# Performance work log

Measured on AMD Instinct MI355X. Metric: run time of the kernel, lower is better.

The kernel has to match this reference:

```python
import jax, jax.numpy as jnp
import numpy as np

HS = 4096
NIN = 17   # RFSIZE*RFSIZE + ADDINPUT + NBACTIONS = 9 + 4 + 4
NACT = 4


def setup_inputs() -> dict:
    key = jax.random.key(0)
    ks = jax.random.split(key, 10)
    return {
        "inputs": jax.random.normal(ks[0], (1, NIN), jnp.float32),
        "hidden": jax.random.normal(ks[1], (1, HS), jnp.float32) * 0.1,
        "hebb": jnp.zeros((HS, HS), jnp.float32),
        "et": jnp.zeros((HS, HS), jnp.float32),
        "pw": jnp.zeros((HS, HS), jnp.float32),
        # i2h Linear(17 -> hs)
        "i2h_w": jax.random.normal(ks[2], (HS, NIN), jnp.float32) * (1.0 / np.sqrt(NIN)),
        "i2h_b": jax.random.normal(ks[3], (HS,), jnp.float32) * 0.01,
        # plastic recurrent params: 0.01 * rand, eta = 0.01 * ones(1)
        "w": 0.01 * jax.random.uniform(ks[4], (HS, HS), jnp.float32),
        "alpha": 0.01 * jax.random.uniform(ks[5], (HS, HS), jnp.float32),
        "eta": 0.01 * jnp.ones((1,), jnp.float32),
        # output heads
        "h2o_w": jax.random.normal(ks[6], (NACT, HS), jnp.float32) * (1.0 / np.sqrt(HS)),
        "h2o_b": jax.random.normal(ks[7], (NACT,), jnp.float32) * 0.01,
        "h2v_w": jax.random.normal(ks[8], (1, HS), jnp.float32) * (1.0 / np.sqrt(HS)),
        "h2v_b": jax.random.normal(ks[9], (1,), jnp.float32) * 0.01,
    }


def reference(inputs, hidden, hebb, et, pw,
              i2h_w, i2h_b, w, alpha, eta,
              h2o_w, h2o_b, h2v_w, h2v_b):
    # type='plastic', rule='hebb', clp=0, addpw=0
    # hactiv = tanh(i2h(inputs) + hidden @ (w + alpha * hebb))
    pre = inputs @ i2h_w.T + i2h_b + hidden @ (w + alpha * hebb)  # [1, HS]
    hactiv = jnp.tanh(pre)
    activout = hactiv @ h2o_w.T + h2o_b   # [1, NBACTIONS]
    valueout = hactiv @ h2v_w.T + h2v_b   # [1, 1]
    # deltahebb = outer(hidden[0], hactiv[0])  (batch 1, matches torch.bmm(...)[0])
    deltahebb = hidden[0][:, None] * hactiv[0][None, :]  # [HS, HS]
    hebb_new = (1.0 - eta) * hebb + eta * deltahebb       # eta shape (1,) broadcasts
    # hidden <- hactiv; et, pw untouched for this type
    return activout, valueout, hactiv, hebb_new, et, pw
```

## Files before the change

### kernel.cpp

```cpp
#include <hip/hip_runtime.h>
#include <math.h>

#define HS 4096
#define NIN 17
#define ROW_CHUNKS 512
#define ROWS_PER_CHUNK (HS / ROW_CHUNKS)

__global__ __launch_bounds__(256) void matvec_partial_k(
    const float* __restrict__ hidden, const float* __restrict__ w,
    const float* __restrict__ alpha, const float* __restrict__ hebb,
    float* __restrict__ partial) {
  const int j4 = blockIdx.x * blockDim.x + threadIdx.x;
  const int row0 = blockIdx.y * ROWS_PER_CHUNK;
  const size_t base = (size_t)row0 * (HS / 4) + j4;
  const float4* wp = reinterpret_cast<const float4*>(w) + base;
  const float4* ap = reinterpret_cast<const float4*>(alpha) + base;
  const float4* bp = reinterpret_cast<const float4*>(hebb) + base;
  float4 acc = make_float4(0.f, 0.f, 0.f, 0.f);
#pragma unroll
  for (int r = 0; r < ROWS_PER_CHUNK; ++r) {
    const float h = hidden[row0 + r];
    const float4 wv = wp[(size_t)r * (HS / 4)];
    const float4 av = ap[(size_t)r * (HS / 4)];
    const float4 bv = bp[(size_t)r * (HS / 4)];
    acc.x = fmaf(h, fmaf(av.x, bv.x, wv.x), acc.x);
    acc.y = fmaf(h, fmaf(av.y, bv.y, wv.y), acc.y);
    acc.z = fmaf(h, fmaf(av.z, bv.z, wv.z), acc.z);
    acc.w = fmaf(h, fmaf(av.w, bv.w, wv.w), acc.w);
  }
  reinterpret_cast<float4*>(partial)[(size_t)blockIdx.y * (HS / 4) + j4] = acc;
}

__global__ __launch_bounds__(256) void finalize_k(
    const float* __restrict__ partial, const float* __restrict__ inputs,
    const float* __restrict__ i2h_w, const float* __restrict__ i2h_b,
    float* __restrict__ out_hactiv) {
  const int j = blockIdx.x * blockDim.x + threadIdx.x;
  float s = i2h_b[j];
#pragma unroll
  for (int k = 0; k < NIN; ++k) s = fmaf(inputs[k], i2h_w[j * NIN + k], s);
  float r = 0.f;
  for (int c = 0; c < ROW_CHUNKS; ++c) r += partial[(size_t)c * HS + j];
  out_hactiv[j] = tanhf(s + r);
}

__global__ __launch_bounds__(256) void heads_k(
    const float* __restrict__ hactiv, const float* __restrict__ h2o_w,
    const float* __restrict__ h2o_b, const float* __restrict__ h2v_w,
    const float* __restrict__ h2v_b, float* __restrict__ out) {
  const int r = blockIdx.x;
  const float* wrow = (r < 4) ? (h2o_w + (size_t)r * HS) : h2v_w;
  float s = 0.f;
  for (int j = threadIdx.x; j < HS; j += 256) s = fmaf(hactiv[j], wrow[j], s);
  __shared__ float red[256];
  red[threadIdx.x] = s;
  __syncthreads();
  for (int off = 128; off > 0; off >>= 1) {
    if (threadIdx.x < off) red[threadIdx.x] += red[threadIdx.x + off];
    __syncthreads();
  }
  if (threadIdx.x == 0) {
    const float b = (r < 4) ? h2o_b[r] : h2v_b[0];
    out[r] = red[0] + b;
  }
}

__global__ __launch_bounds__(256) void elementwise_k(
    const float* __restrict__ hebb, const float* __restrict__ hidden,
    const float* __restrict__ hactiv, const float* __restrict__ eta,
    const float* __restrict__ et, const float* __restrict__ pw,
    float* __restrict__ out_hebb, float* __restrict__ out_et,
    float* __restrict__ out_pw) {
  const unsigned NSQ = (unsigned)HS * HS;
  const unsigned stride = gridDim.x * blockDim.x;
  const unsigned tid = blockIdx.x * blockDim.x + threadIdx.x;
  const float e = eta[0];
  const float one_m_e = 1.f - e;
  for (unsigned t = tid; t < NSQ; t += stride) {
    const float hi = hidden[t >> 12];
    const float ha = hactiv[t & (HS - 1)];
    out_hebb[t] = fmaf(one_m_e, hebb[t], e * hi * ha);
  }
  for (unsigned t = tid; t < NSQ; t += stride) out_et[t] = et[t];
  for (unsigned t = tid; t < NSQ; t += stride) out_pw[t] = pw[t];
}

extern "C" void kernel_launch(void* const* d_in, const int* in_sizes, int n_in,
                              void* d_out, int out_size, void* d_ws, size_t ws_size,
                              hipStream_t stream) {
  const float* inputs = (const float*)d_in[0];
  const float* hidden = (const float*)d_in[1];
  const float* hebb   = (const float*)d_in[2];
  const float* et     = (const float*)d_in[3];
  const float* pw     = (const float*)d_in[4];
  const float* i2h_w  = (const float*)d_in[5];
  const float* i2h_b  = (const float*)d_in[6];
  const float* w      = (const float*)d_in[7];
  const float* alpha  = (const float*)d_in[8];
  const float* eta    = (const float*)d_in[9];
  const float* h2o_w  = (const float*)d_in[10];
  const float* h2o_b  = (const float*)d_in[11];
  const float* h2v_w  = (const float*)d_in[12];
  const float* h2v_b  = (const float*)d_in[13];

  float* out = (float*)d_out;
  const size_t NSQ = (size_t)HS * HS;
  float* out_heads  = out;
  float* out_hactiv = out + 5;
  float* out_hebb   = out + 5 + HS;
  float* out_et     = out_hebb + NSQ;
  float* out_pw     = out_et + NSQ;

  const size_t need = (size_t)ROW_CHUNKS * HS * sizeof(float);
  float* partial = (ws_size >= need) ? (float*)d_ws
                                     : (out_hebb + 3 );

  hipLaunchKernelGGL(matvec_partial_k, dim3(HS / 4 / 256, ROW_CHUNKS), dim3(256),
                     0, stream, hidden, w, alpha, hebb, partial);
  hipLaunchKernelGGL(finalize_k, dim3(HS / 256), dim3(256), 0, stream,
                     partial, inputs, i2h_w, i2h_b, out_hactiv);
  hipLaunchKernelGGL(heads_k, dim3(5), dim3(256), 0, stream,
                     out_hactiv, h2o_w, h2o_b, h2v_w, h2v_b, out_heads);
  hipLaunchKernelGGL(elementwise_k, dim3(2048), dim3(256), 0, stream,
                     hebb, hidden, out_hactiv, eta, et, pw,
                     out_hebb, out_et, out_pw);
}
```

Before: 488.5 us.

## Fuse et/pw copies into matvec kernel, use nontemporal access, parallelize finalize reduction

Moves the et and pw copy-through into the matvec kernel so those streams overlap with the bandwidth-bound matvec instead of running after it. Adds nontemporal loads and stores for the streams read or written once (w, alpha, et, pw, out_hebb), while hebb keeps normal loads so it may stay in cache for the later hebb update. Changes the finalize step to one 64-lane wavefront per output column that reduces the 512 partials with shuffles, instead of one thread per column summing them serially. The copy mapping relies on the grid covering exactly HS*HS elements at 8192 per block.

```diff
diff --git a/kernel.cpp b/kernel.cpp
--- a/kernel.cpp
+++ b/kernel.cpp
@@ -6,42 +6,66 @@
 #define ROW_CHUNKS 512
 #define ROWS_PER_CHUNK (HS / ROW_CHUNKS)
 
-__global__ __launch_bounds__(256) void matvec_partial_k(
+typedef float vfloat4 __attribute__((ext_vector_type(4)));
+
+__device__ __forceinline__ vfloat4 ntload4(const vfloat4* p) {
+  return __builtin_nontemporal_load(p);
+}
+__device__ __forceinline__ float ntloadf(const float* p) {
+  return __builtin_nontemporal_load(p);
+}
+__device__ __forceinline__ void ntstoref(float* p, float v) {
+  __builtin_nontemporal_store(v, p);
+}
+
+__global__ __launch_bounds__(256) void matvec_copy_k(
     const float* __restrict__ hidden, const float* __restrict__ w,
     const float* __restrict__ alpha, const float* __restrict__ hebb,
-    float* __restrict__ partial) {
+    const float* __restrict__ et, const float* __restrict__ pw,
+    float* __restrict__ partial, float* __restrict__ out_et,
+    float* __restrict__ out_pw) {
   const int j4 = blockIdx.x * blockDim.x + threadIdx.x;
   const int row0 = blockIdx.y * ROWS_PER_CHUNK;
   const size_t base = (size_t)row0 * (HS / 4) + j4;
-  const float4* wp = reinterpret_cast<const float4*>(w) + base;
-  const float4* ap = reinterpret_cast<const float4*>(alpha) + base;
-  const float4* bp = reinterpret_cast<const float4*>(hebb) + base;
-  float4 acc = make_float4(0.f, 0.f, 0.f, 0.f);
+  const vfloat4* wp = reinterpret_cast<const vfloat4*>(w) + base;
+  const vfloat4* ap = reinterpret_cast<const vfloat4*>(alpha) + base;
+  const vfloat4* bp = reinterpret_cast<const vfloat4*>(hebb) + base;
+  vfloat4 acc = (vfloat4)(0.f);
 #pragma unroll
   for (int r = 0; r < ROWS_PER_CHUNK; ++r) {
     const float h = hidden[row0 + r];
-    const float4 wv = wp[(size_t)r * (HS / 4)];
-    const float4 av = ap[(size_t)r * (HS / 4)];
-    const float4 bv = bp[(size_t)r * (HS / 4)];
-    acc.x = fmaf(h, fmaf(av.x, bv.x, wv.x), acc.x);
-    acc.y = fmaf(h, fmaf(av.y, bv.y, wv.y), acc.y);
-    acc.z = fmaf(h, fmaf(av.z, bv.z, wv.z), acc.z);
-    acc.w = fmaf(h, fmaf(av.w, bv.w, wv.w), acc.w);
+    const vfloat4 wv = ntload4(wp + (size_t)r * (HS / 4));
+    const vfloat4 av = ntload4(ap + (size_t)r * (HS / 4));
+    const vfloat4 bv = bp[(size_t)r * (HS / 4)];
+#pragma unroll
+    for (int c = 0; c < 4; ++c)
+      acc[c] = fmaf(h, fmaf(av[c], bv[c], wv[c]), acc[c]);
   }
-  reinterpret_cast<float4*>(partial)[(size_t)blockIdx.y * (HS / 4) + j4] = acc;
+  reinterpret_cast<vfloat4*>(partial)[(size_t)blockIdx.y * (HS / 4) + j4] = acc;
+
+  const size_t cbase = ((size_t)blockIdx.y * gridDim.x + blockIdx.x) * 8192 + threadIdx.x;
+#pragma unroll
+  for (int i = 0; i < 32; ++i) {
+    const size_t t = cbase + (size_t)i * 256;
+    ntstoref(out_et + t, ntloadf(et + t));
+    ntstoref(out_pw + t, ntloadf(pw + t));
+  }
 }
 
-__global__ __launch_bounds__(256) void finalize_k(
+__global__ __launch_bounds__(64) void finalize_k(
     const float* __restrict__ partial, const float* __restrict__ inputs,
     const float* __restrict__ i2h_w, const float* __restrict__ i2h_b,
     float* __restrict__ out_hactiv) {
-  const int j = blockIdx.x * blockDim.x + threadIdx.x;
-  float s = i2h_b[j];
+  const int j = blockIdx.x;
+  const int lane = threadIdx.x;
+  float s = 0.f;
 #pragma unroll
-  for (int k = 0; k < NIN; ++k) s = fmaf(inputs[k], i2h_w[j * NIN + k], s);
-  float r = 0.f;
-  for (int c = 0; c < ROW_CHUNKS; ++c) r += partial[(size_t)c * HS + j];
-  out_hactiv[j] = tanhf(s + r);
+  for (int i = 0; i < ROW_CHUNKS / 64; ++i)
+    s += partial[(size_t)(lane + 64 * i) * HS + j];
+  if (lane < NIN) s = fmaf(inputs[lane], i2h_w[j * NIN + lane], s);
+#pragma unroll
+  for (int off = 32; off > 0; off >>= 1) s += __shfl_down(s, off, 64);
+  if (lane == 0) out_hactiv[j] = tanhf(s + i2h_b[j]);
 }
 
 __global__ __launch_bounds__(256) void heads_k(
@@ -59,30 +83,22 @@
     if (threadIdx.x < off) red[threadIdx.x] += red[threadIdx.x + off];
     __syncthreads();
   }
-  if (threadIdx.x == 0) {
-    const float b = (r < 4) ? h2o_b[r] : h2v_b[0];
-    out[r] = red[0] + b;
-  }
+  if (threadIdx.x == 0) out[r] = red[0] + ((r < 4) ? h2o_b[r] : h2v_b[0]);
 }
 
-__global__ __launch_bounds__(256) void elementwise_k(
+__global__ __launch_bounds__(256) void hebb_k(
     const float* __restrict__ hebb, const float* __restrict__ hidden,
     const float* __restrict__ hactiv, const float* __restrict__ eta,
-    const float* __restrict__ et, const float* __restrict__ pw,
-    float* __restrict__ out_hebb, float* __restrict__ out_et,
-    float* __restrict__ out_pw) {
+    float* __restrict__ out_hebb) {
   const unsigned NSQ = (unsigned)HS * HS;
   const unsigned stride = gridDim.x * blockDim.x;
-  const unsigned tid = blockIdx.x * blockDim.x + threadIdx.x;
   const float e = eta[0];
   const float one_m_e = 1.f - e;
-  for (unsigned t = tid; t < NSQ; t += stride) {
+  for (unsigned t = blockIdx.x * blockDim.x + threadIdx.x; t < NSQ; t += stride) {
     const float hi = hidden[t >> 12];
     const float ha = hactiv[t & (HS - 1)];
-    out_hebb[t] = fmaf(one_m_e, hebb[t], e * hi * ha);
+    ntstoref(out_hebb + t, fmaf(one_m_e, hebb[t], e * hi * ha));
   }
-  for (unsigned t = tid; t < NSQ; t += stride) out_et[t] = et[t];
-  for (unsigned t = tid; t < NSQ; t += stride) out_pw[t] = pw[t];
 }
 
 extern "C" void kernel_launch(void* const* d_in, const int* in_sizes, int n_in,
@@ -115,13 +131,13 @@
   float* partial = (ws_size >= need) ? (float*)d_ws
                                      : (out_hebb + 3 );
 
-  hipLaunchKernelGGL(matvec_partial_k, dim3(HS / 4 / 256, ROW_CHUNKS), dim3(256),
-                     0, stream, hidden, w, alpha, hebb, partial);
-  hipLaunchKernelGGL(finalize_k, dim3(HS / 256), dim3(256), 0, stream,
+  hipLaunchKernelGGL(matvec_copy_k, dim3(HS / 4 / 256, ROW_CHUNKS), dim3(256),
+                     0, stream, hidden, w, alpha, hebb, et, pw,
+                     partial, out_et, out_pw);
+  hipLaunchKernelGGL(finalize_k, dim3(HS), dim3(64), 0, stream,
                      partial, inputs, i2h_w, i2h_b, out_hactiv);
   hipLaunchKernelGGL(heads_k, dim3(5), dim3(256), 0, stream,
                      out_hactiv, h2o_w, h2o_b, h2v_w, h2v_b, out_heads);
-  hipLaunchKernelGGL(elementwise_k, dim3(2048), dim3(256), 0, stream,
-                     hebb, hidden, out_hactiv, eta, et, pw,
-                     out_hebb, out_et, out_pw);
+  hipLaunchKernelGGL(hebb_k, dim3(2048), dim3(256), 0, stream,
+                     hebb, hidden, out_hactiv, eta, out_hebb);
 }
```

Result: no change. 481.8 us (-1.4%).
